# Optimization experiments

Measured on AMD Instinct MI355X. Metric: run time of the kernel, lower is better.

Reference implementation:

```python
import jax, jax.numpy as jnp
import numpy as np

HEADS = 8


def setup_inputs() -> dict:
    key = jax.random.key(0)
    ks = jax.random.split(key, 5)
    B, C, H, W = 2, 256, 48, 48
    s = 0.02
    return {
        "ct": jax.random.normal(ks[0], (B, C, H, W), jnp.float32),
        "us": jax.random.normal(ks[1], (B, C, H, W), jnp.float32),
        "w_qkv_ct": jax.random.normal(ks[2], (3 * C, C), jnp.float32) * s,
        "w_qkv_us": jax.random.normal(ks[3], (3 * C, C), jnp.float32) * s,
        "w_proj": jax.random.normal(ks[4], (C, 2 * C), jnp.float32) * s,
        "b_proj": jnp.zeros((C,), jnp.float32),
    }


def _heads_view(x, B, H, W):
    # [B, C, H, W] -> [B, heads, HW, dh]
    C = x.shape[1]
    return x.reshape(B, HEADS, C // HEADS, H * W).transpose(0, 1, 3, 2)


def _cross_attn(q, k, v, scale):
    # q,k,v: [B, heads, HW, dh]
    attn = jax.nn.softmax(jnp.einsum("bhnd,bhmd->bhnm", q, k) * scale, axis=-1)
    return jnp.einsum("bhnm,bhmd->bhnd", attn, v)


def reference(ct, us, w_qkv_ct, w_qkv_us, w_proj, b_proj):
    B, C, H, W = ct.shape
    dh = C // HEADS
    scale = dh ** (-0.5)

    # 1x1 convs as channel GEMMs
    qkv1 = jnp.einsum("oc,bchw->bohw", w_qkv_ct, ct)
    qkv2 = jnp.einsum("oc,bchw->bohw", w_qkv_us, us)
    q1, k1, v1 = jnp.split(qkv1, 3, axis=1)
    q2, k2, v2 = jnp.split(qkv2, 3, axis=1)

    # CT queries attend to US keys/values
    o1 = _cross_attn(_heads_view(q1, B, H, W), _heads_view(k2, B, H, W),
                     _heads_view(v2, B, H, W), scale)
    # US queries attend to CT keys/values
    o2 = _cross_attn(_heads_view(q2, B, H, W), _heads_view(k1, B, H, W),
                     _heads_view(v1, B, H, W), scale)

    # [B, heads, HW, dh] -> [B, C, H, W]
    out1 = o1.transpose(0, 1, 3, 2).reshape(B, C, H, W)
    out2 = o2.transpose(0, 1, 3, 2).reshape(B, C, H, W)

    fused = jnp.concatenate([ct + out1, us + out2], axis=1)
    return jnp.einsum("oc,bchw->bohw", w_proj, fused) + b_proj[None, :, None, None]
```

## Files before the change

kernel.cpp:

```cpp
#include <hip/hip_runtime.h>
#include <hip/hip_bf16.h>
#include <math.h>

#define HW   2304
#define CCH  256

#define QSCALE 0.25504368686637270f

typedef short short8 __attribute__((ext_vector_type(8)));
typedef float f32x4  __attribute__((ext_vector_type(4)));

__device__ inline unsigned short f2bf(float f) {
    union { float f; unsigned u; } v; v.f = f;
    unsigned r = v.u + 0x7FFF + ((v.u >> 16) & 1);
    return (unsigned short)(r >> 16);
}
__device__ inline unsigned pkbf2(float a, float b) {
    float2 f; f.x = a; f.y = b;
    union { __hip_bfloat162 h; unsigned u; } c;
    c.h = __float22bfloat162_rn(f);
    return c.u;
}
__device__ inline unsigned pktrunc(float a, float b) {
    return __builtin_amdgcn_perm(__builtin_bit_cast(unsigned, b),
                                 __builtin_bit_cast(unsigned, a), 0x07060302u);
}

__device__ __forceinline__ void prep_unit(
    int u, int t,
    const float* __restrict__ ct, const float* __restrict__ us,
    const float* __restrict__ w1, const float* __restrict__ w2,
    const float* __restrict__ w3,
    unsigned short* __restrict__ xT,
    unsigned short* __restrict__ wb1, unsigned short* __restrict__ wb2,
    unsigned short* __restrict__ w3b,
    unsigned short* __restrict__ Ts)
{
    if (u >= 576) {
        const int v_ = u - 576;
        int z, base;
        if (v_ < 192)      { z = 0; base = v_ * 1024; }
        else if (v_ < 384) { z = 1; base = (v_ - 192) * 1024; }
        else               { z = 2; base = (v_ - 384) * 1024; }
        const float* s = (z == 0) ? w1 : (z == 1) ? w2 : w3;
        unsigned short* d = (z == 0) ? wb1 : (z == 1) ? wb2 : w3b;
        const int i = base + t * 4;
        const float4 v4 = *(const float4*)&s[i];
        const float sc = (z < 2 && i < 65536) ? QSCALE : 1.f;
        uint2 p; p.x = pkbf2(v4.x * sc, v4.y * sc); p.y = pkbf2(v4.z * sc, v4.w * sc);
        *(uint2*)&d[i] = p;
        return;
    }
    const int pt = u % 36, rest = u / 36, ctile = rest & 3, z = rest >> 2;
    const float* __restrict__ src = ((z >> 1) ? us : ct) + (size_t)(z & 1) * CCH * HW;
    unsigned short* __restrict__ dst = xT + (size_t)z * HW * 256;
    const int p0 = pt * 64, c0 = ctile * 64;
    __syncthreads();
#pragma unroll
    for (int r = 0; r < 4; r++) {
        const int c = (t >> 4) + 16 * r;
        const float4 v4 = *(const float4*)&src[(size_t)(c0 + c) * HW + p0 + (t & 15) * 4];
        Ts[((t & 15) * 4 + 0) * 72 + c] = f2bf(v4.x);
        Ts[((t & 15) * 4 + 1) * 72 + c] = f2bf(v4.y);
        Ts[((t & 15) * 4 + 2) * 72 + c] = f2bf(v4.z);
        Ts[((t & 15) * 4 + 3) * 72 + c] = f2bf(v4.w);
    }
    __syncthreads();
    const int p = t >> 2, c8 = (t & 3) * 16;
    const short8 a  = *(const short8*)&Ts[p * 72 + c8];
    const short8 b8 = *(const short8*)&Ts[p * 72 + c8 + 8];
    *(short8*)&dst[(size_t)(p0 + p) * 256 + c0 + c8]     = a;
    *(short8*)&dst[(size_t)(p0 + p) * 256 + c0 + c8 + 8] = b8;
}

__device__ __forceinline__ void qkv_unit(
    int ptile, int otile, int z, int t,
    const unsigned short* __restrict__ xT,
    const unsigned short* __restrict__ wb1, const unsigned short* __restrict__ wb2,
    unsigned short* __restrict__ qkvT1, unsigned short* __restrict__ qkvT2,
    unsigned short* __restrict__ vdm1,  unsigned short* __restrict__ vdm2,
    unsigned short* __restrict__ Ws, unsigned short* __restrict__ Xs)
{
    const int inp = z >> 1, b = z & 1;
    const unsigned short* __restrict__ X = xT + (size_t)(inp * 2 + b) * HW * 256;
    const unsigned short* __restrict__ W = inp ? wb2 : wb1;
    unsigned short* __restrict__ qT = (inp ? qkvT2 : qkvT1) + (size_t)b * HW * 512;
    unsigned short* __restrict__ vd = (inp ? vdm2 : vdm1) + (size_t)b * CCH * HW;
    const int p0 = ptile * 64, o0 = otile * 64;
    const int w = t >> 6, lane = t & 63, quad = lane >> 4, m = lane & 15;
    const int sr = t >> 3, sc = t & 7;

    f32x4 acc[4] = {{0,0,0,0},{0,0,0,0},{0,0,0,0},{0,0,0,0}};
    for (int k0 = 0; k0 < 256; k0 += 64) {
        const short8 wv0 = *(const short8*)&W[(size_t)(o0 + sr) * 256 + k0 + sc * 8];
        const short8 wv1 = *(const short8*)&W[(size_t)(o0 + 32 + sr) * 256 + k0 + sc * 8];
        const short8 xv0 = *(const short8*)&X[(size_t)(p0 + sr) * 256 + k0 + sc * 8];
        const short8 xv1 = *(const short8*)&X[(size_t)(p0 + 32 + sr) * 256 + k0 + sc * 8];
        __syncthreads();
        *(short8*)&Ws[sr * 72 + sc * 8] = wv0;
        *(short8*)&Ws[(32 + sr) * 72 + sc * 8] = wv1;
        *(short8*)&Xs[sr * 72 + sc * 8] = xv0;
        *(short8*)&Xs[(32 + sr) * 72 + sc * 8] = xv1;
        __syncthreads();
#pragma unroll
        for (int kc2 = 0; kc2 < 2; kc2++) {
            const short8 af = *(const short8*)&Ws[(w * 16 + m) * 72 + kc2 * 32 + quad * 8];
#pragma unroll
            for (int pg = 0; pg < 4; pg++) {
                const short8 bf = *(const short8*)&Xs[(pg * 16 + m) * 72 + kc2 * 32 + quad * 8];
                acc[pg] = __builtin_amdgcn_mfma_f32_16x16x32_bf16(af, bf, acc[pg], 0, 0, 0);
            }
        }
    }
    __syncthreads();
    if (o0 < 512) {
#pragma unroll
        for (int pg = 0; pg < 4; pg++) {
            uint2 pk; pk.x = pkbf2(acc[pg][0], acc[pg][1]); pk.y = pkbf2(acc[pg][2], acc[pg][3]);
            *(uint2*)&Ws[(pg * 16 + m) * 72 + w * 16 + quad * 4] = pk;
        }
        __syncthreads();
        const int pr = t >> 2, cc = t & 3;
        const uint4 d0 = *(const uint4*)&Ws[pr * 72 + cc * 16];
        const uint4 d1 = *(const uint4*)&Ws[pr * 72 + cc * 16 + 8];
        *(uint4*)&qT[(size_t)(p0 + pr) * 512 + o0 + cc * 16]     = d0;
        *(uint4*)&qT[(size_t)(p0 + pr) * 512 + o0 + cc * 16 + 8] = d1;
    } else {
#pragma unroll
        for (int pg = 0; pg < 4; pg++)
#pragma unroll
            for (int r = 0; r < 4; r++)
                Ws[(w * 16 + quad * 4 + r) * 72 + pg * 16 + m] = f2bf(acc[pg][r]);
        __syncthreads();
        const int dr = t >> 2, cc = t & 3;
        const uint4 d0 = *(const uint4*)&Ws[dr * 72 + cc * 16];
        const uint4 d1 = *(const uint4*)&Ws[dr * 72 + cc * 16 + 8];
        *(uint4*)&vd[(size_t)(o0 - 512 + dr) * HW + p0 + cc * 16]     = d0;
        *(uint4*)&vd[(size_t)(o0 - 512 + dr) * HW + p0 + cc * 16 + 8] = d1;
    }
}

__device__ __forceinline__ void proj_unit(
    int ptile, int otile, int t,
    const unsigned short* __restrict__ w3b, const unsigned short* __restrict__ fusedT,
    const float* __restrict__ bias, float* __restrict__ out,
    unsigned short* __restrict__ Ws, unsigned short* __restrict__ Xs)
{
    const int p0 = ptile * 64, o0 = otile * 64;
    const int w = t >> 6, lane = t & 63, quad = lane >> 4, m = lane & 15;
    const int sr = t >> 3, sc = t & 7;

    f32x4 acc[4] = {{0,0,0,0},{0,0,0,0},{0,0,0,0},{0,0,0,0}};
    for (int k0 = 0; k0 < 512; k0 += 64) {
        const short8 wv0 = *(const short8*)&w3b[(size_t)(o0 + sr) * 512 + k0 + sc * 8];
        const short8 wv1 = *(const short8*)&w3b[(size_t)(o0 + 32 + sr) * 512 + k0 + sc * 8];
        const short8 xv0 = *(const short8*)&fusedT[(size_t)(p0 + sr) * 512 + k0 + sc * 8];
        const short8 xv1 = *(const short8*)&fusedT[(size_t)(p0 + 32 + sr) * 512 + k0 + sc * 8];
        __syncthreads();
        *(short8*)&Ws[sr * 72 + sc * 8] = wv0;
        *(short8*)&Ws[(32 + sr) * 72 + sc * 8] = wv1;
        *(short8*)&Xs[sr * 72 + sc * 8] = xv0;
        *(short8*)&Xs[(32 + sr) * 72 + sc * 8] = xv1;
        __syncthreads();
#pragma unroll
        for (int kc2 = 0; kc2 < 2; kc2++) {
            const short8 af = *(const short8*)&Ws[(w * 16 + m) * 72 + kc2 * 32 + quad * 8];
#pragma unroll
            for (int pg = 0; pg < 4; pg++) {
                const short8 bf = *(const short8*)&Xs[(pg * 16 + m) * 72 + kc2 * 32 + quad * 8];
                acc[pg] = __builtin_amdgcn_mfma_f32_16x16x32_bf16(af, bf, acc[pg], 0, 0, 0);
            }
        }
    }
    const int b = (p0 >= HW) ? 1 : 0;
    const int pl0 = p0 - b * HW;
    float* __restrict__ ob = out + (size_t)b * CCH * HW;
    float b4[4];
#pragma unroll
    for (int r = 0; r < 4; r++) b4[r] = bias[o0 + w * 16 + quad * 4 + r];
#pragma unroll
    for (int pg = 0; pg < 4; pg++)
#pragma unroll
        for (int r = 0; r < 4; r++)
            ob[(size_t)(o0 + w * 16 + quad * 4 + r) * HW + pl0 + pg * 16 + m]
                = acc[pg][r] + b4[r];
}

__global__ __launch_bounds__(256, 4) void prep_k(
    const float* __restrict__ ct, const float* __restrict__ us,
    const float* __restrict__ w1, const float* __restrict__ w2,
    const float* __restrict__ w3,
    unsigned short* __restrict__ xT,
    unsigned short* __restrict__ b1, unsigned short* __restrict__ b2,
    unsigned short* __restrict__ b3)
{
    __shared__ __align__(16) unsigned short Ts[64 * 72];
    prep_unit(blockIdx.x, threadIdx.x, ct, us, w1, w2, w3, xT, b1, b2, b3, Ts);
}

__global__ __launch_bounds__(256, 4) void qkv_k(
    const unsigned short* __restrict__ xT,
    const unsigned short* __restrict__ wb1, const unsigned short* __restrict__ wb2,
    unsigned short* __restrict__ qkvT1, unsigned short* __restrict__ qkvT2,
    unsigned short* __restrict__ vdm1,  unsigned short* __restrict__ vdm2)
{
    __shared__ __align__(16) unsigned short Ws[64 * 72];
    __shared__ __align__(16) unsigned short Xs[64 * 72];
    qkv_unit(blockIdx.x, blockIdx.y, blockIdx.z, threadIdx.x,
             xT, wb1, wb2, qkvT1, qkvT2, vdm1, vdm2, Ws, Xs);
}

__global__ __launch_bounds__(256, 4) void proj_k(
    const unsigned short* __restrict__ w3b, const unsigned short* __restrict__ fusedT,
    const float* __restrict__ bias, float* __restrict__ out)
{
    __shared__ __align__(16) unsigned short Ws[64 * 72];
    __shared__ __align__(16) unsigned short Xs[64 * 72];
    proj_unit(blockIdx.x, blockIdx.y, threadIdx.x, w3b, fusedT, bias, out, Ws, Xs);
}

__global__ __launch_bounds__(256, 3) void attn_k(
    const unsigned short* __restrict__ qkvT1, const unsigned short* __restrict__ qkvT2,
    const unsigned short* __restrict__ vdm1,  const unsigned short* __restrict__ vdm2,
    const float* __restrict__ ct, const float* __restrict__ us,
    unsigned short* __restrict__ fusedT)
{
    const int dir = blockIdx.z, b = blockIdx.y >> 3, h = blockIdx.y & 7;
    const unsigned short* __restrict__ Qt = (dir ? qkvT2 : qkvT1) + (size_t)b * HW * 512;
    const unsigned short* __restrict__ Kt = (dir ? qkvT1 : qkvT2) + (size_t)b * HW * 512
                                            + 256 + h * 32;
    const unsigned short* __restrict__ Vd = (dir ? vdm1 : vdm2) + ((size_t)b * CCH + h * 32) * HW;
    const float* __restrict__ src = (dir ? us : ct) + ((size_t)b * CCH + h * 32) * HW;

    const int t = threadIdx.x, w = t >> 6, lane = t & 63, quad = lane >> 4, m = lane & 15;

    __shared__ __align__(16) unsigned short Ks[128 * 32];
    __shared__ __align__(16) unsigned short Vs[32 * 136];

    const int pq0 = blockIdx.x * 128 + w * 32 + m;
    const int pq1 = pq0 + 16;
    const short8 qf0 = *(const short8*)&Qt[(size_t)pq0 * 512 + h * 32 + quad * 8];
    const short8 qf1 = *(const short8*)&Qt[(size_t)pq1 * 512 + h * 32 + quad * 8];

    f32x4 acc00 = {0,0,0,0}, acc10 = {0,0,0,0};
    f32x4 acc01 = {0,0,0,0}, acc11 = {0,0,0,0};
    f32x4 accl0 = {0,0,0,0}, accl1 = {0,0,0,0};
    const short ONE = (short)0x3F80;
    const short8 ones = {ONE,ONE,ONE,ONE,ONE,ONE,ONE,ONE};

    const int kj0 = t >> 2, kcs = t & 3;
    const int pcK = kcs ^ (((kj0 >> 1) & 1) | (((kj0 >> 3) & 1) << 1));
    const int vr0 = t >> 4, vcs = t & 15;
    const int g2m = ((m >> 1) & 1) | (((m >> 2) & 1) << 1);
    const unsigned short* __restrict__ ksb =
        &Ks[((m >> 2) * 8 + (m & 3)) * 32 + (quad ^ g2m) * 8];
    const unsigned short* __restrict__ vsb = &Vs[m * 136 + quad * 8];

    short8 ka = *(const short8*)&Kt[(size_t)kj0 * 512 + kcs * 8];
    short8 kb = *(const short8*)&Kt[(size_t)(kj0 + 64) * 512 + kcs * 8];
    short8 va = *(const short8*)&Vd[(size_t)vr0 * HW + vcs * 8];
    short8 vb = *(const short8*)&Vd[(size_t)(vr0 + 16) * HW + vcs * 8];

    for (int j0 = 0; j0 < HW; j0 += 128) {
        __syncthreads();
        *(short8*)&Ks[kj0 * 32 + pcK * 8] = ka;
        *(short8*)&Ks[(kj0 + 64) * 32 + pcK * 8] = kb;
        *(short8*)&Vs[vr0 * 136 + vcs * 8] = va;
        *(short8*)&Vs[(vr0 + 16) * 136 + vcs * 8] = vb;
        const int jn = (j0 + 128 < HW) ? j0 + 128 : 0;
        ka = *(const short8*)&Kt[(size_t)(jn + kj0) * 512 + kcs * 8];
        kb = *(const short8*)&Kt[(size_t)(jn + kj0 + 64) * 512 + kcs * 8];
        va = *(const short8*)&Vd[(size_t)vr0 * HW + jn + vcs * 8];
        vb = *(const short8*)&Vd[(size_t)(vr0 + 16) * HW + jn + vcs * 8];
        __syncthreads();

        uint4 pw4a[4], pw4b[4];
#pragma unroll
        for (int f = 0; f < 8; f++) {
            const short8 kf = *(const short8*)(ksb + ((f >> 1) * 32 + (f & 1) * 4) * 32);
            const f32x4 z = {0,0,0,0};
            const f32x4 S0 = __builtin_amdgcn_mfma_f32_16x16x32_bf16(kf, qf0, z, 0, 0, 0);
            const f32x4 S1 = __builtin_amdgcn_mfma_f32_16x16x32_bf16(kf, qf1, z, 0, 0, 0);
            const unsigned pa0 = pktrunc(__builtin_amdgcn_exp2f(S0[0]), __builtin_amdgcn_exp2f(S0[1]));
            const unsigned pa1 = pktrunc(__builtin_amdgcn_exp2f(S0[2]), __builtin_amdgcn_exp2f(S0[3]));
            const unsigned pb0 = pktrunc(__builtin_amdgcn_exp2f(S1[0]), __builtin_amdgcn_exp2f(S1[1]));
            const unsigned pb1 = pktrunc(__builtin_amdgcn_exp2f(S1[2]), __builtin_amdgcn_exp2f(S1[3]));
            if ((f & 1) == 0) {
                pw4a[f >> 1].x = pa0; pw4a[f >> 1].y = pa1;
                pw4b[f >> 1].x = pb0; pw4b[f >> 1].y = pb1;
            } else {
                pw4a[f >> 1].z = pa0; pw4a[f >> 1].w = pa1;
                pw4b[f >> 1].z = pb0; pw4b[f >> 1].w = pb1;
            }
        }

#pragma unroll
        for (int kt = 0; kt < 4; kt++) {
            const short8 pf0 = __builtin_bit_cast(short8, pw4a[kt]);
            const short8 pf1 = __builtin_bit_cast(short8, pw4b[kt]);
            const short8 vf0 = *(const short8*)(vsb + kt * 32);
            const short8 vf1 = *(const short8*)(vsb + 16 * 136 + kt * 32);
            acc00 = __builtin_amdgcn_mfma_f32_16x16x32_bf16(vf0, pf0, acc00, 0, 0, 0);
            acc10 = __builtin_amdgcn_mfma_f32_16x16x32_bf16(vf1, pf0, acc10, 0, 0, 0);
            acc01 = __builtin_amdgcn_mfma_f32_16x16x32_bf16(vf0, pf1, acc01, 0, 0, 0);
            acc11 = __builtin_amdgcn_mfma_f32_16x16x32_bf16(vf1, pf1, acc11, 0, 0, 0);
            accl0 = __builtin_amdgcn_mfma_f32_16x16x32_bf16(ones, pf0, accl0, 0, 0, 0);
            accl1 = __builtin_amdgcn_mfma_f32_16x16x32_bf16(ones, pf1, accl1, 0, 0, 0);
        }
    }

    const float inv0 = 1.f / accl0[0];
    const float inv1 = 1.f / accl1[0];

    const int cb = dir * 256 + h * 32, d0 = quad * 4;
#pragma unroll
    for (int qi = 0; qi < 2; qi++) {
        const int pq = qi ? pq1 : pq0;
        const float inv = qi ? inv1 : inv0;
        const f32x4 aL = qi ? acc01 : acc00;
        const f32x4 aH = qi ? acc11 : acc10;
        unsigned short* __restrict__ fT = fusedT + ((size_t)b * HW + pq) * 512 + cb + d0;
        uint2 s0, s1;
        s0.x = pkbf2(aL[0] * inv + src[(size_t)(d0 + 0) * HW + pq],
                     aL[1] * inv + src[(size_t)(d0 + 1) * HW + pq]);
        s0.y = pkbf2(aL[2] * inv + src[(size_t)(d0 + 2) * HW + pq],
                     aL[3] * inv + src[(size_t)(d0 + 3) * HW + pq]);
        s1.x = pkbf2(aH[0] * inv + src[(size_t)(16 + d0 + 0) * HW + pq],
                     aH[1] * inv + src[(size_t)(16 + d0 + 1) * HW + pq]);
        s1.y = pkbf2(aH[2] * inv + src[(size_t)(16 + d0 + 2) * HW + pq],
                     aH[3] * inv + src[(size_t)(16 + d0 + 3) * HW + pq]);
        *(uint2*)&fT[0]  = s0;
        *(uint2*)&fT[16] = s1;
    }
}

extern "C" void kernel_launch(void* const* d_in, const int* in_sizes, int n_in,
                              void* d_out, int out_size, void* d_ws, size_t ws_size,
                              hipStream_t stream)
{
    const float* ct       = (const float*)d_in[0];
    const float* us       = (const float*)d_in[1];
    const float* w_qkv_ct = (const float*)d_in[2];
    const float* w_qkv_us = (const float*)d_in[3];
    const float* w_proj   = (const float*)d_in[4];
    const float* b_proj   = (const float*)d_in[5];
    float* out = (float*)d_out;

    unsigned short* wb1   = (unsigned short*)d_ws;
    unsigned short* wb2   = wb1 + (size_t)768 * 256;
    unsigned short* w3b   = wb2 + (size_t)768 * 256;
    unsigned short* xT    = w3b + (size_t)256 * 512;
    unsigned short* qkvT1 = xT    + (size_t)4 * HW * 256;
    unsigned short* qkvT2 = qkvT1 + (size_t)2 * HW * 512;
    unsigned short* vdm1  = qkvT2 + (size_t)2 * HW * 512;
    unsigned short* vdm2  = vdm1  + (size_t)2 * CCH * HW;
    unsigned short* fusedT= vdm2  + (size_t)2 * CCH * HW;

    prep_k<<<dim3(1088), 256, 0, stream>>>(ct, us, w_qkv_ct, w_qkv_us, w_proj,
                                           xT, wb1, wb2, w3b);
    qkv_k <<<dim3(36, 12, 4), 256, 0, stream>>>(xT, wb1, wb2, qkvT1, qkvT2, vdm1, vdm2);
    attn_k<<<dim3(18, 16, 2), 256, 0, stream>>>(qkvT1, qkvT2, vdm1, vdm2, ct, us, fusedT);
    proj_k<<<dim3(72, 4), 256, 0, stream>>>(w3b, fusedT, b_proj, out);
}
```

Baseline: 126.9 us.

## Split attention over key range and merge partial results in new kernel

The attention kernel now splits the key dimension into two halves, doubling the grid from 576 to 1152 blocks. Each half writes unnormalized bf16 partial outputs plus row sums, and a new merge kernel combines them, normalizes, adds the residual and writes fusedT. The merge works without max tracking, which suggests the softmax here skips max subtraction. Launch bounds for attention go from 3 to 4 waves. The cost is an extra launch, extra global traffic for partials, and bf16 rounding of the partials before the merge.

```diff
diff --git a/kernel.cpp b/kernel.cpp
--- a/kernel.cpp
+++ b/kernel.cpp
@@ -14,6 +14,10 @@
     union { float f; unsigned u; } v; v.f = f;
     unsigned r = v.u + 0x7FFF + ((v.u >> 16) & 1);
     return (unsigned short)(r >> 16);
+}
+__device__ inline float bf2f(unsigned short u) {
+    union { unsigned u; float f; } v; v.u = ((unsigned)u) << 16;
+    return v.f;
 }
 __device__ inline unsigned pkbf2(float a, float b) {
     float2 f; f.x = a; f.y = b;
@@ -26,24 +30,23 @@
                                  __builtin_bit_cast(unsigned, a), 0x07060302u);
 }
 
-__device__ __forceinline__ void prep_unit(
-    int u, int t,
+__global__ __launch_bounds__(256, 4) void prep_k(
     const float* __restrict__ ct, const float* __restrict__ us,
     const float* __restrict__ w1, const float* __restrict__ w2,
     const float* __restrict__ w3,
     unsigned short* __restrict__ xT,
-    unsigned short* __restrict__ wb1, unsigned short* __restrict__ wb2,
-    unsigned short* __restrict__ w3b,
-    unsigned short* __restrict__ Ts)
-{
-    if (u >= 576) {
-        const int v_ = u - 576;
+    unsigned short* __restrict__ b1, unsigned short* __restrict__ b2,
+    unsigned short* __restrict__ b3)
+{
+    const int bx = blockIdx.x, t = threadIdx.x;
+    if (bx >= 576) {
+        const int v_ = bx - 576;
         int z, base;
         if (v_ < 192)      { z = 0; base = v_ * 1024; }
         else if (v_ < 384) { z = 1; base = (v_ - 192) * 1024; }
         else               { z = 2; base = (v_ - 384) * 1024; }
         const float* s = (z == 0) ? w1 : (z == 1) ? w2 : w3;
-        unsigned short* d = (z == 0) ? wb1 : (z == 1) ? wb2 : w3b;
+        unsigned short* d = (z == 0) ? b1 : (z == 1) ? b2 : b3;
         const int i = base + t * 4;
         const float4 v4 = *(const float4*)&s[i];
         const float sc = (z < 2 && i < 65536) ? QSCALE : 1.f;
@@ -51,11 +54,11 @@
         *(uint2*)&d[i] = p;
         return;
     }
-    const int pt = u % 36, rest = u / 36, ctile = rest & 3, z = rest >> 2;
+    const int pt = bx % 36, rest = bx / 36, ctile = rest & 3, z = rest >> 2;
     const float* __restrict__ src = ((z >> 1) ? us : ct) + (size_t)(z & 1) * CCH * HW;
     unsigned short* __restrict__ dst = xT + (size_t)z * HW * 256;
     const int p0 = pt * 64, c0 = ctile * 64;
-    __syncthreads();
+    __shared__ __align__(16) unsigned short Ts[64 * 72];
 #pragma unroll
     for (int r = 0; r < 4; r++) {
         const int c = (t >> 4) + 16 * r;
@@ -73,21 +76,21 @@
     *(short8*)&dst[(size_t)(p0 + p) * 256 + c0 + c8 + 8] = b8;
 }
 
-__device__ __forceinline__ void qkv_unit(
-    int ptile, int otile, int z, int t,
+__global__ __launch_bounds__(256, 4) void qkv_k(
     const unsigned short* __restrict__ xT,
     const unsigned short* __restrict__ wb1, const unsigned short* __restrict__ wb2,
     unsigned short* __restrict__ qkvT1, unsigned short* __restrict__ qkvT2,
-    unsigned short* __restrict__ vdm1,  unsigned short* __restrict__ vdm2,
-    unsigned short* __restrict__ Ws, unsigned short* __restrict__ Xs)
-{
-    const int inp = z >> 1, b = z & 1;
+    unsigned short* __restrict__ vdm1,  unsigned short* __restrict__ vdm2)
+{
+    const int inp = blockIdx.z >> 1, b = blockIdx.z & 1;
     const unsigned short* __restrict__ X = xT + (size_t)(inp * 2 + b) * HW * 256;
     const unsigned short* __restrict__ W = inp ? wb2 : wb1;
     unsigned short* __restrict__ qT = (inp ? qkvT2 : qkvT1) + (size_t)b * HW * 512;
     unsigned short* __restrict__ vd = (inp ? vdm2 : vdm1) + (size_t)b * CCH * HW;
-    const int p0 = ptile * 64, o0 = otile * 64;
-    const int w = t >> 6, lane = t & 63, quad = lane >> 4, m = lane & 15;
+    const int p0 = blockIdx.x * 64, o0 = blockIdx.y * 64;
+    __shared__ __align__(16) unsigned short Ws[64 * 72];
+    __shared__ __align__(16) unsigned short Xs[64 * 72];
+    const int t = threadIdx.x, w = t >> 6, lane = t & 63, quad = lane >> 4, m = lane & 15;
     const int sr = t >> 3, sc = t & 7;
 
     f32x4 acc[4] = {{0,0,0,0},{0,0,0,0},{0,0,0,0},{0,0,0,0}};
@@ -140,97 +143,18 @@
     }
 }
 
-__device__ __forceinline__ void proj_unit(
-    int ptile, int otile, int t,
-    const unsigned short* __restrict__ w3b, const unsigned short* __restrict__ fusedT,
-    const float* __restrict__ bias, float* __restrict__ out,
-    unsigned short* __restrict__ Ws, unsigned short* __restrict__ Xs)
-{
-    const int p0 = ptile * 64, o0 = otile * 64;
-    const int w = t >> 6, lane = t & 63, quad = lane >> 4, m = lane & 15;
-    const int sr = t >> 3, sc = t & 7;
-
-    f32x4 acc[4] = {{0,0,0,0},{0,0,0,0},{0,0,0,0},{0,0,0,0}};
-    for (int k0 = 0; k0 < 512; k0 += 64) {
-        const short8 wv0 = *(const short8*)&w3b[(size_t)(o0 + sr) * 512 + k0 + sc * 8];
-        const short8 wv1 = *(const short8*)&w3b[(size_t)(o0 + 32 + sr) * 512 + k0 + sc * 8];
-        const short8 xv0 = *(const short8*)&fusedT[(size_t)(p0 + sr) * 512 + k0 + sc * 8];
-        const short8 xv1 = *(const short8*)&fusedT[(size_t)(p0 + 32 + sr) * 512 + k0 + sc * 8];
-        __syncthreads();
-        *(short8*)&Ws[sr * 72 + sc * 8] = wv0;
-        *(short8*)&Ws[(32 + sr) * 72 + sc * 8] = wv1;
-        *(short8*)&Xs[sr * 72 + sc * 8] = xv0;
-        *(short8*)&Xs[(32 + sr) * 72 + sc * 8] = xv1;
-        __syncthreads();
-#pragma unroll
-        for (int kc2 = 0; kc2 < 2; kc2++) {
-            const short8 af = *(const short8*)&Ws[(w * 16 + m) * 72 + kc2 * 32 + quad * 8];
-#pragma unroll
-            for (int pg = 0; pg < 4; pg++) {
-                const short8 bf = *(const short8*)&Xs[(pg * 16 + m) * 72 + kc2 * 32 + quad * 8];
-                acc[pg] = __builtin_amdgcn_mfma_f32_16x16x32_bf16(af, bf, acc[pg], 0, 0, 0);
-            }
-        }
-    }
-    const int b = (p0 >= HW) ? 1 : 0;
-    const int pl0 = p0 - b * HW;
-    float* __restrict__ ob = out + (size_t)b * CCH * HW;
-    float b4[4];
-#pragma unroll
-    for (int r = 0; r < 4; r++) b4[r] = bias[o0 + w * 16 + quad * 4 + r];
-#pragma unroll
-    for (int pg = 0; pg < 4; pg++)
-#pragma unroll
-        for (int r = 0; r < 4; r++)
-            ob[(size_t)(o0 + w * 16 + quad * 4 + r) * HW + pl0 + pg * 16 + m]
-                = acc[pg][r] + b4[r];
-}
-
-__global__ __launch_bounds__(256, 4) void prep_k(
-    const float* __restrict__ ct, const float* __restrict__ us,
-    const float* __restrict__ w1, const float* __restrict__ w2,
-    const float* __restrict__ w3,
-    unsigned short* __restrict__ xT,
-    unsigned short* __restrict__ b1, unsigned short* __restrict__ b2,
-    unsigned short* __restrict__ b3)
-{
-    __shared__ __align__(16) unsigned short Ts[64 * 72];
-    prep_unit(blockIdx.x, threadIdx.x, ct, us, w1, w2, w3, xT, b1, b2, b3, Ts);
-}
-
-__global__ __launch_bounds__(256, 4) void qkv_k(
-    const unsigned short* __restrict__ xT,
-    const unsigned short* __restrict__ wb1, const unsigned short* __restrict__ wb2,
-    unsigned short* __restrict__ qkvT1, unsigned short* __restrict__ qkvT2,
-    unsigned short* __restrict__ vdm1,  unsigned short* __restrict__ vdm2)
-{
-    __shared__ __align__(16) unsigned short Ws[64 * 72];
-    __shared__ __align__(16) unsigned short Xs[64 * 72];
-    qkv_unit(blockIdx.x, blockIdx.y, blockIdx.z, threadIdx.x,
-             xT, wb1, wb2, qkvT1, qkvT2, vdm1, vdm2, Ws, Xs);
-}
-
-__global__ __launch_bounds__(256, 4) void proj_k(
-    const unsigned short* __restrict__ w3b, const unsigned short* __restrict__ fusedT,
-    const float* __restrict__ bias, float* __restrict__ out)
-{
-    __shared__ __align__(16) unsigned short Ws[64 * 72];
-    __shared__ __align__(16) unsigned short Xs[64 * 72];
-    proj_unit(blockIdx.x, blockIdx.y, threadIdx.x, w3b, fusedT, bias, out, Ws, Xs);
-}
-
-__global__ __launch_bounds__(256, 3) void attn_k(
+__global__ __launch_bounds__(256, 4) void attn_k(
     const unsigned short* __restrict__ qkvT1, const unsigned short* __restrict__ qkvT2,
     const unsigned short* __restrict__ vdm1,  const unsigned short* __restrict__ vdm2,
-    const float* __restrict__ ct, const float* __restrict__ us,
-    unsigned short* __restrict__ fusedT)
-{
-    const int dir = blockIdx.z, b = blockIdx.y >> 3, h = blockIdx.y & 7;
+    unsigned short* __restrict__ pOb, float* __restrict__ pL)
+{
+    const int dir = blockIdx.z >> 1, s = blockIdx.z & 1;
+    const int b = blockIdx.y >> 3, h = blockIdx.y & 7;
+    const int inst = (dir * 2 + b) * 8 + h;
     const unsigned short* __restrict__ Qt = (dir ? qkvT2 : qkvT1) + (size_t)b * HW * 512;
     const unsigned short* __restrict__ Kt = (dir ? qkvT1 : qkvT2) + (size_t)b * HW * 512
                                             + 256 + h * 32;
     const unsigned short* __restrict__ Vd = (dir ? vdm1 : vdm2) + ((size_t)b * CCH + h * 32) * HW;
-    const float* __restrict__ src = (dir ? us : ct) + ((size_t)b * CCH + h * 32) * HW;
 
     const int t = threadIdx.x, w = t >> 6, lane = t & 63, quad = lane >> 4, m = lane & 15;
 
@@ -256,18 +180,19 @@
         &Ks[((m >> 2) * 8 + (m & 3)) * 32 + (quad ^ g2m) * 8];
     const unsigned short* __restrict__ vsb = &Vs[m * 136 + quad * 8];
 
-    short8 ka = *(const short8*)&Kt[(size_t)kj0 * 512 + kcs * 8];
-    short8 kb = *(const short8*)&Kt[(size_t)(kj0 + 64) * 512 + kcs * 8];
-    short8 va = *(const short8*)&Vd[(size_t)vr0 * HW + vcs * 8];
-    short8 vb = *(const short8*)&Vd[(size_t)(vr0 + 16) * HW + vcs * 8];
-
-    for (int j0 = 0; j0 < HW; j0 += 128) {
+    const int jlo = s * 1152, jhi = jlo + 1152;
+    short8 ka = *(const short8*)&Kt[(size_t)(jlo + kj0) * 512 + kcs * 8];
+    short8 kb = *(const short8*)&Kt[(size_t)(jlo + kj0 + 64) * 512 + kcs * 8];
+    short8 va = *(const short8*)&Vd[(size_t)vr0 * HW + jlo + vcs * 8];
+    short8 vb = *(const short8*)&Vd[(size_t)(vr0 + 16) * HW + jlo + vcs * 8];
+
+    for (int j0 = jlo; j0 < jhi; j0 += 128) {
         __syncthreads();
         *(short8*)&Ks[kj0 * 32 + pcK * 8] = ka;
         *(short8*)&Ks[(kj0 + 64) * 32 + pcK * 8] = kb;
         *(short8*)&Vs[vr0 * 136 + vcs * 8] = va;
         *(short8*)&Vs[(vr0 + 16) * 136 + vcs * 8] = vb;
-        const int jn = (j0 + 128 < HW) ? j0 + 128 : 0;
+        const int jn = (j0 + 128 < jhi) ? j0 + 128 : jlo;
         ka = *(const short8*)&Kt[(size_t)(jn + kj0) * 512 + kcs * 8];
         kb = *(const short8*)&Kt[(size_t)(jn + kj0 + 64) * 512 + kcs * 8];
         va = *(const short8*)&Vd[(size_t)vr0 * HW + jn + vcs * 8];
@@ -293,7 +218,6 @@
                 pw4b[f >> 1].z = pb0; pw4b[f >> 1].w = pb1;
             }
         }
-
 #pragma unroll
         for (int kt = 0; kt < 4; kt++) {
             const short8 pf0 = __builtin_bit_cast(short8, pw4a[kt]);
@@ -309,29 +233,93 @@
         }
     }
 
-    const float inv0 = 1.f / accl0[0];
-    const float inv1 = 1.f / accl1[0];
-
-    const int cb = dir * 256 + h * 32, d0 = quad * 4;
+    unsigned short* __restrict__ po = pOb + (size_t)(inst * 2 + s) * 32 * HW;
+    float* __restrict__ pl = pL + (size_t)(inst * 2 + s) * HW;
 #pragma unroll
     for (int qi = 0; qi < 2; qi++) {
         const int pq = qi ? pq1 : pq0;
-        const float inv = qi ? inv1 : inv0;
         const f32x4 aL = qi ? acc01 : acc00;
         const f32x4 aH = qi ? acc11 : acc10;
-        unsigned short* __restrict__ fT = fusedT + ((size_t)b * HW + pq) * 512 + cb + d0;
-        uint2 s0, s1;
-        s0.x = pkbf2(aL[0] * inv + src[(size_t)(d0 + 0) * HW + pq],
-                     aL[1] * inv + src[(size_t)(d0 + 1) * HW + pq]);
-        s0.y = pkbf2(aL[2] * inv + src[(size_t)(d0 + 2) * HW + pq],
-                     aL[3] * inv + src[(size_t)(d0 + 3) * HW + pq]);
-        s1.x = pkbf2(aH[0] * inv + src[(size_t)(16 + d0 + 0) * HW + pq],
-                     aH[1] * inv + src[(size_t)(16 + d0 + 1) * HW + pq]);
-        s1.y = pkbf2(aH[2] * inv + src[(size_t)(16 + d0 + 2) * HW + pq],
-                     aH[3] * inv + src[(size_t)(16 + d0 + 3) * HW + pq]);
-        *(uint2*)&fT[0]  = s0;
-        *(uint2*)&fT[16] = s1;
-    }
+#pragma unroll
+        for (int r = 0; r < 4; r++) {
+            po[(size_t)(quad * 4 + r) * HW + pq]      = f2bf(aL[r]);
+            po[(size_t)(16 + quad * 4 + r) * HW + pq] = f2bf(aH[r]);
+        }
+        if (quad == 0) pl[pq] = qi ? accl1[0] : accl0[0];
+    }
+}
+
+__global__ __launch_bounds__(256, 8) void merge_k(
+    const unsigned short* __restrict__ pOb, const float* __restrict__ pL,
+    const float* __restrict__ ct, const float* __restrict__ us,
+    unsigned short* __restrict__ fusedT)
+{
+    const int inst = blockIdx.y;
+    const int dir = inst >> 4, b = (inst >> 3) & 1, h = inst & 7;
+    const unsigned short* __restrict__ p0 = pOb + (size_t)(inst * 2 + 0) * 32 * HW;
+    const unsigned short* __restrict__ p1 = pOb + (size_t)(inst * 2 + 1) * 32 * HW;
+    const float* __restrict__ src = (dir ? us : ct) + ((size_t)b * CCH + h * 32) * HW;
+    const int t = threadIdx.x, q = blockIdx.x * 64 + (t & 63), dg = (t >> 6) * 8;
+
+    const float inv = 1.f / (pL[(size_t)(inst * 2 + 0) * HW + q] +
+                             pL[(size_t)(inst * 2 + 1) * HW + q]);
+    float v[8];
+#pragma unroll
+    for (int i = 0; i < 8; i++) {
+        const int d = dg + i;
+        v[i] = (bf2f(p0[(size_t)d * HW + q]) + bf2f(p1[(size_t)d * HW + q])) * inv
+               + src[(size_t)d * HW + q];
+    }
+    uint4 pk;
+    pk.x = pkbf2(v[0], v[1]); pk.y = pkbf2(v[2], v[3]);
+    pk.z = pkbf2(v[4], v[5]); pk.w = pkbf2(v[6], v[7]);
+    *(uint4*)&fusedT[((size_t)b * HW + q) * 512 + dir * 256 + h * 32 + dg] = pk;
+}
+
+__global__ __launch_bounds__(256, 4) void proj_k(
+    const unsigned short* __restrict__ w3b, const unsigned short* __restrict__ fusedT,
+    const float* __restrict__ bias, float* __restrict__ out)
+{
+    const int p0 = blockIdx.x * 64, o0 = blockIdx.y * 64;
+    __shared__ __align__(16) unsigned short Ws[64 * 72];
+    __shared__ __align__(16) unsigned short Xs[64 * 72];
+    const int t = threadIdx.x, w = t >> 6, lane = t & 63, quad = lane >> 4, m = lane & 15;
+    const int sr = t >> 3, sc = t & 7;
+
+    f32x4 acc[4] = {{0,0,0,0},{0,0,0,0},{0,0,0,0},{0,0,0,0}};
+    for (int k0 = 0; k0 < 512; k0 += 64) {
+        const short8 wv0 = *(const short8*)&w3b[(size_t)(o0 + sr) * 512 + k0 + sc * 8];
+        const short8 wv1 = *(const short8*)&w3b[(size_t)(o0 + 32 + sr) * 512 + k0 + sc * 8];
+        const short8 xv0 = *(const short8*)&fusedT[(size_t)(p0 + sr) * 512 + k0 + sc * 8];
+        const short8 xv1 = *(const short8*)&fusedT[(size_t)(p0 + 32 + sr) * 512 + k0 + sc * 8];
+        __syncthreads();
+        *(short8*)&Ws[sr * 72 + sc * 8] = wv0;
+        *(short8*)&Ws[(32 + sr) * 72 + sc * 8] = wv1;
+        *(short8*)&Xs[sr * 72 + sc * 8] = xv0;
+        *(short8*)&Xs[(32 + sr) * 72 + sc * 8] = xv1;
+        __syncthreads();
+#pragma unroll
+        for (int kc2 = 0; kc2 < 2; kc2++) {
+            const short8 af = *(const short8*)&Ws[(w * 16 + m) * 72 + kc2 * 32 + quad * 8];
+#pragma unroll
+            for (int pg = 0; pg < 4; pg++) {
+                const short8 bf = *(const short8*)&Xs[(pg * 16 + m) * 72 + kc2 * 32 + quad * 8];
+                acc[pg] = __builtin_amdgcn_mfma_f32_16x16x32_bf16(af, bf, acc[pg], 0, 0, 0);
+            }
+        }
+    }
+    const int b = (p0 >= HW) ? 1 : 0;
+    const int pl0 = p0 - b * HW;
+    float* __restrict__ ob = out + (size_t)b * CCH * HW;
+    float b4[4];
+#pragma unroll
+    for (int r = 0; r < 4; r++) b4[r] = bias[o0 + w * 16 + quad * 4 + r];
+#pragma unroll
+    for (int pg = 0; pg < 4; pg++)
+#pragma unroll
+        for (int r = 0; r < 4; r++)
+            ob[(size_t)(o0 + w * 16 + quad * 4 + r) * HW + pl0 + pg * 16 + m]
+                = acc[pg][r] + b4[r];
 }
 
 extern "C" void kernel_launch(void* const* d_in, const int* in_sizes, int n_in,
@@ -355,10 +343,13 @@
     unsigned short* vdm1  = qkvT2 + (size_t)2 * HW * 512;
     unsigned short* vdm2  = vdm1  + (size_t)2 * CCH * HW;
     unsigned short* fusedT= vdm2  + (size_t)2 * CCH * HW;
-
-    prep_k<<<dim3(1088), 256, 0, stream>>>(ct, us, w_qkv_ct, w_qkv_us, w_proj,
-                                           xT, wb1, wb2, w3b);
-    qkv_k <<<dim3(36, 12, 4), 256, 0, stream>>>(xT, wb1, wb2, qkvT1, qkvT2, vdm1, vdm2);
-    attn_k<<<dim3(18, 16, 2), 256, 0, stream>>>(qkvT1, qkvT2, vdm1, vdm2, ct, us, fusedT);
-    proj_k<<<dim3(72, 4), 256, 0, stream>>>(w3b, fusedT, b_proj, out);
-}
+    unsigned short* pOb   = fusedT + (size_t)2 * HW * 512;
+    float*          pL    = (float*)(pOb + (size_t)64 * 32 * HW);
+
+    prep_k <<<dim3(1088), 256, 0, stream>>>(ct, us, w_qkv_ct, w_qkv_us, w_proj,
+                                            xT, wb1, wb2, w3b);
+    qkv_k  <<<dim3(36, 12, 4), 256, 0, stream>>>(xT, wb1, wb2, qkvT1, qkvT2, vdm1, vdm2);
+    attn_k <<<dim3(18, 16, 4), 256, 0, stream>>>(qkvT1, qkvT2, vdm1, vdm2, pOb, pL);
+    merge_k<<<dim3(36, 32), 256, 0, stream>>>(pOb, pL, ct, us, fusedT);
+    proj_k <<<dim3(72, 4), 256, 0, stream>>>(w3b, fusedT, b_proj, out);
+}
```

Measured after the change: 128.3 us. About the same (+1.0%).
